# Kernel tuning notes

Measured on AMD Instinct MI355X. Metric: run time of the kernel, lower is better.

Reference implementation:

```python
import jax, jax.numpy as jnp
import numpy as np

H = 1024          # hid_dim
SEQ = 149         # input tokens (cls makes 150)
B = 128           # batch
WIN = 20          # local attention band half-width (hard-coded in module)


def _pe_table(n, d):
    # ConstantPE with period=1: position = 2*pi*arange(n)
    pos = 2.0 * np.pi * np.arange(n, dtype=np.float64)[:, None]
    div = np.exp(np.arange(0, d, 2, dtype=np.float64) * (-np.log(10000.0) / d))
    pe = np.zeros((n, d), dtype=np.float32)
    pe[:, 0::2] = np.sin(pos * div)
    pe[:, 1::2] = np.cos(pos * div)
    return jnp.asarray(pe)


def _band_mask(n, w=WIN):
    # True where attention is DISALLOWED (matches src_mask == 1)
    r = np.arange(n)[:, None]
    c = np.arange(n)[None, :]
    allowed = (c >= np.maximum(r - w, 0)) & (c < r + w)
    allowed[0, :] = True  # cls row attends everywhere
    return jnp.asarray(~allowed)


def _layer_norm(x, g, b, eps=1e-5):
    m = jnp.mean(x, axis=-1, keepdims=True)
    v = jnp.var(x, axis=-1, keepdims=True)
    return (x - m) * jax.lax.rsqrt(v + eps) * g + b


def setup_inputs() -> dict:
    key = jax.random.key(0)
    ks = jax.random.split(key, 8)
    s = 0.02
    return {
        "z": jax.random.normal(ks[0], (SEQ, B, H), jnp.float32),
        "cls_token": jax.random.normal(ks[1], (1, H), jnp.float32),
        "ln_g": jnp.ones((H,), jnp.float32),
        "ln_b": jnp.zeros((H,), jnp.float32),
        "w_qkv": jax.random.normal(ks[2], (H, 3 * H), jnp.float32) * s,
        "b_qkv": jnp.zeros((3 * H,), jnp.float32),
        "w_o": jax.random.normal(ks[3], (H, H), jnp.float32) * s,
        "b_o": jnp.zeros((H,), jnp.float32),
        "w_m1": jax.random.normal(ks[4], (H, H), jnp.float32) * s,
        "b_m1": jnp.zeros((H,), jnp.float32),
        "w_m2": jax.random.normal(ks[5], (H, H), jnp.float32) * s,
        "b_m2": jnp.zeros((H,), jnp.float32),
    }


def reference(z, cls_token, ln_g, ln_b, w_qkv, b_qkv, w_o, b_o, w_m1, b_m1, w_m2, b_m2):
    S1 = z.shape[0] + 1  # tokens incl. cls
    pe = _pe_table(S1, H)          # (S1, H)
    neg_mask = _band_mask(S1)      # (S1, S1) bool, True = masked

    x = jnp.swapaxes(z, 0, 1)                                   # (B, S, H)
    cls = jnp.broadcast_to(cls_token[None], (x.shape[0], 1, H))  # (B, 1, H)
    x = jnp.concatenate([cls, x], axis=1)                        # (B, S1, H)
    x = _layer_norm(x + pe[None], ln_g, ln_b)

    qkv = x @ w_qkv + b_qkv
    q, k, v = jnp.split(qkv, 3, axis=-1)

    attn = jnp.einsum("bqh,bkh->bqk", q, k) / jnp.sqrt(jnp.float32(H))
    attn = jnp.where(neg_mask[None], jnp.float32(-1e10), attn)
    attn = jax.nn.softmax(attn, axis=-1)

    sa = jnp.einsum("bqk,bkh->bqh", attn, v) @ w_o + b_o
    zsa = _layer_norm(x + sa, ln_g, ln_b)

    mlp = jax.nn.gelu(zsa @ w_m1 + b_m1, approximate=False) @ w_m2 + b_m2
    out = zsa + mlp
    return jnp.swapaxes(out, 0, 1)  # (S1, B, H)
```

## Files before the change

### kernel.cpp

```cpp
#include <hip/hip_runtime.h>
#include <math.h>

#define HD 1024
#define S1 150
#define BATCH 128
#define MTOK (S1 * BATCH)
#define WIN 20
#define QKVLD (3 * HD)

typedef unsigned short bf16_t;
typedef short s16x8 __attribute__((ext_vector_type(8)));
typedef float f32x4 __attribute__((ext_vector_type(4)));

__device__ __forceinline__ float bf2f(unsigned int u16) {
  return __uint_as_float(u16 << 16);
}
__device__ __forceinline__ unsigned short f2bf(float f) {
  unsigned int u = __float_as_uint(f);
  u += 0x7fff + ((u >> 16) & 1);
  return (unsigned short)(u >> 16);
}

__device__ __forceinline__ float wave_sum(float v) {
#pragma unroll
  for (int o = 32; o; o >>= 1) v += __shfl_down(v, o, 64);
  return v;
}

__device__ __forceinline__ void gload_lds16(const bf16_t* g, bf16_t* l) {
  __builtin_amdgcn_global_load_lds(
      (const __attribute__((address_space(1))) unsigned int*)(unsigned long long)(const void*)g,
      (__attribute__((address_space(3))) unsigned int*)(unsigned int)(unsigned long long)(void*)l,
      16, 0, 0);
}

__global__ __launch_bounds__(256) void transpose_kernel(
    const float* __restrict__ W, bf16_t* __restrict__ WT, int K, int N) {
  __shared__ float t[32][33];
  int n0 = blockIdx.x * 32, k0 = blockIdx.y * 32;
  int tx = threadIdx.x, ty = threadIdx.y;
#pragma unroll
  for (int i = 0; i < 4; i++)
    t[ty + i * 8][tx] = W[(size_t)(k0 + ty + i * 8) * N + n0 + tx];
  __syncthreads();
#pragma unroll
  for (int i = 0; i < 4; i++)
    WT[(size_t)(n0 + ty + i * 8) * K + k0 + tx] = f2bf(t[tx][ty + i * 8]);
}

__global__ void pe_kernel(float* __restrict__ pe) {
  int s = blockIdx.x;
  double pos = 6.283185307179586476925286766559 * (double)s;
  for (int p = threadIdx.x; p < HD / 2; p += blockDim.x) {
    double dv = exp((double)(2 * p) * (-9.210340371976184 / (double)HD));
    double a = pos * dv;
    pe[s * HD + 2 * p] = (float)sin(a);
    pe[s * HD + 2 * p + 1] = (float)cos(a);
  }
}

__global__ __launch_bounds__(256) void build_x_kernel(
    const float* __restrict__ z, const float* __restrict__ cls,
    const float* __restrict__ pe, const float* __restrict__ g,
    const float* __restrict__ be, bf16_t* __restrict__ x) {
  int t = blockIdx.x;
  int b = t / S1, s = t % S1;
  const float* src = (s == 0) ? cls : (z + ((size_t)(s - 1) * BATCH + b) * HD);
  const float* pr = pe + (size_t)s * HD;
  int tid = threadIdx.x;
  float vals[4];
  float sum = 0.f, sq = 0.f;
#pragma unroll
  for (int i = 0; i < 4; i++) {
    int h = tid + i * 256;
    float v = src[h] + pr[h];
    vals[i] = v;
    sum += v;
    sq += v * v;
  }
  __shared__ float shs[4], shq[4];
  __shared__ float sm, sr;
  sum = wave_sum(sum);
  sq = wave_sum(sq);
  int wave = tid >> 6, lane = tid & 63;
  if (!lane) { shs[wave] = sum; shq[wave] = sq; }
  __syncthreads();
  if (!tid) {
    float S = shs[0] + shs[1] + shs[2] + shs[3];
    float Q = shq[0] + shq[1] + shq[2] + shq[3];
    float mean = S * (1.f / HD);
    float var = Q * (1.f / HD) - mean * mean;
    sm = mean;
    sr = rsqrtf(var + 1e-5f);
  }
  __syncthreads();
  float mean = sm, rstd = sr;
  bf16_t* xr = x + (size_t)t * HD;
#pragma unroll
  for (int i = 0; i < 4; i++) {
    int h = tid + i * 256;
    xr[h] = f2bf((vals[i] - mean) * rstd * g[h] + be[h]);
  }
}

__global__ __launch_bounds__(256) void ln_residual_kernel(
    const bf16_t* __restrict__ a, const bf16_t* __restrict__ r,
    const float* __restrict__ g, const float* __restrict__ be,
    bf16_t* __restrict__ out) {
  int t = blockIdx.x;
  int tid = threadIdx.x;
  const bf16_t* ar = a + (size_t)t * QKVLD;
  const bf16_t* rr = r + (size_t)t * HD;
  float vals[4];
  float sum = 0.f, sq = 0.f;
#pragma unroll
  for (int i = 0; i < 4; i++) {
    int h = tid + i * 256;
    float v = bf2f(ar[h]) + bf2f(rr[h]);
    vals[i] = v;
    sum += v;
    sq += v * v;
  }
  __shared__ float shs[4], shq[4];
  __shared__ float sm, sr;
  sum = wave_sum(sum);
  sq = wave_sum(sq);
  int wave = tid >> 6, lane = tid & 63;
  if (!lane) { shs[wave] = sum; shq[wave] = sq; }
  __syncthreads();
  if (!tid) {
    float S = shs[0] + shs[1] + shs[2] + shs[3];
    float Q = shq[0] + shq[1] + shq[2] + shq[3];
    float mean = S * (1.f / HD);
    float var = Q * (1.f / HD) - mean * mean;
    sm = mean;
    sr = rsqrtf(var + 1e-5f);
  }
  __syncthreads();
  float mean = sm, rstd = sr;
  bf16_t* outp = out + (size_t)t * QKVLD;
#pragma unroll
  for (int i = 0; i < 4; i++) {
    int h = tid + i * 256;
    outp[h] = f2bf((vals[i] - mean) * rstd * g[h] + be[h]);
  }
}

template <int EPI>
__global__ __launch_bounds__(512, 2) void gemm256_kernel(
    const bf16_t* __restrict__ A, int lda, const bf16_t* __restrict__ WT,
    const float* __restrict__ bias, bf16_t* __restrict__ C, int ldc,
    const bf16_t* __restrict__ res, float* __restrict__ outf) {
  constexpr int NT = 32;
  __shared__ bf16_t ALDS[4 * 8192];
  __shared__ bf16_t BLDS[4 * 8192];
  int tid = threadIdx.x;
  int w = tid >> 6, lane = tid & 63;
  int wm = w >> 2, wn = w & 3;
  int m0 = blockIdx.y * 256, n0 = blockIdx.x * 256;

  int sr = lane >> 2;
  int scol = ((lane & 3) ^ ((sr >> 1) & 3)) * 8;
  const bf16_t* gA = A + (size_t)(m0 + w * 16 + sr) * lda + scol;
  const bf16_t* gB = WT + (size_t)(n0 + w * 16 + sr) * 1024 + scol;
  bf16_t* lA = ALDS + w * 512;
  bf16_t* lB = BLDS + w * 512;
  size_t ldh = (size_t)128 * lda;

#define STAGE_A(tt)                                                   \
  do {                                                                \
    int bb_ = (tt) & 3;                                               \
    gload_lds16(gA + (tt) * 32, lA + bb_ * 8192);                     \
    gload_lds16(gA + ldh + (tt) * 32, lA + bb_ * 8192 + 4096);        \
  } while (0)
#define STAGE_B(tt)                                                   \
  do {                                                                \
    int bb_ = (tt) & 3;                                               \
    gload_lds16(gB + (tt) * 32, lB + bb_ * 8192);                     \
    gload_lds16(gB + 131072 + (tt) * 32, lB + bb_ * 8192 + 4096);     \
  } while (0)

  int frow = lane & 15;
  int fslot = ((lane >> 4) ^ ((frow >> 1) & 3)) * 8;
  int aoff[8], boff[4];
#pragma unroll
  for (int i = 0; i < 8; i++) aoff[i] = (wm * 8 + i) * 512 + frow * 32 + fslot;
#pragma unroll
  for (int j = 0; j < 4; j++) boff[j] = (wn * 4 + j) * 512 + frow * 32 + fslot;

  f32x4 acc[8][4] = {};

  STAGE_A(0); STAGE_B(0);
  STAGE_A(1); STAGE_B(1);
  STAGE_A(2); STAGE_B(2);

  for (int t = 0; t < NT; ++t) {
    const bf16_t* Ab = ALDS + (t & 3) * 8192;
    const bf16_t* Bb = BLDS + (t & 3) * 8192;
    asm volatile("s_waitcnt vmcnt(8)" ::: "memory");
    __builtin_amdgcn_s_barrier();
    asm volatile("" ::: "memory");
    bool pf = (t + 3 < NT);
    if (pf) STAGE_A(t + 3);
    s16x8 af[8], b0, b1;
#pragma unroll
    for (int i = 0; i < 8; i++) af[i] = *(const s16x8*)(Ab + aoff[i]);
    b0 = *(const s16x8*)(Bb + boff[0]);
    b1 = *(const s16x8*)(Bb + boff[1]);
    __builtin_amdgcn_s_setprio(1);
#pragma unroll
    for (int i = 0; i < 8; i++) {
      acc[i][0] = __builtin_amdgcn_mfma_f32_16x16x32_bf16(af[i], b0, acc[i][0], 0, 0, 0);
      acc[i][1] = __builtin_amdgcn_mfma_f32_16x16x32_bf16(af[i], b1, acc[i][1], 0, 0, 0);
    }
    __builtin_amdgcn_s_setprio(0);
    if (pf) STAGE_B(t + 3);
    b0 = *(const s16x8*)(Bb + boff[2]);
    b1 = *(const s16x8*)(Bb + boff[3]);
    __builtin_amdgcn_s_setprio(1);
#pragma unroll
    for (int i = 0; i < 8; i++) {
      acc[i][2] = __builtin_amdgcn_mfma_f32_16x16x32_bf16(af[i], b0, acc[i][2], 0, 0, 0);
      acc[i][3] = __builtin_amdgcn_mfma_f32_16x16x32_bf16(af[i], b1, acc[i][3], 0, 0, 0);
    }
    __builtin_amdgcn_s_setprio(0);
  }
#undef STAGE_A
#undef STAGE_B

  int erow = (lane >> 4) * 4, ecol = lane & 15;
#pragma unroll
  for (int j = 0; j < 4; j++) {
    int n = n0 + wn * 64 + j * 16 + ecol;
    float bb = bias[n];
#pragma unroll
    for (int i = 0; i < 8; i++) {
      int mb = m0 + wm * 128 + i * 16 + erow;
#pragma unroll
      for (int r = 0; r < 4; r++) {
        int m = mb + r;
        float v = acc[i][j][r] + bb;
        if (EPI == 1) v = 0.5f * v * (1.f + erff(v * 0.7071067811865476f));
        if (EPI == 2) {
          int b = m / S1, s = m % S1;
          v += bf2f(res[(size_t)m * QKVLD + n]);
          outf[((size_t)s * BATCH + b) * HD + n] = v;
        } else {
          C[(size_t)m * ldc + n] = f2bf(v);
        }
      }
    }
  }
}

__global__ __launch_bounds__(256) void attn_tile_kernel(bf16_t* __restrict__ qkv) {
  int g = blockIdx.x;
  int xcd = g & 7, tt0 = g >> 3;
  int qt = tt0 % 5, b = xcd + 8 * (tt0 / 5);
  int q0 = qt * 32;

  int lo_col = (qt == 0) ? 0 : (q0 - 20);
  int hi_col = (qt == 0) ? 150 : ((q0 + 51 < 150) ? q0 + 51 : 150);
  int ct0 = lo_col >> 5;
  int cth = (hi_col + 31) >> 5;
  int NCT = cth - ct0;
  int W = NCT * 32;
  int NSUB = NCT * 2;
  int NT = 2 * NSUB;
  int T = NT >> 2;

  __shared__ bf16_t Qs[2 * 32 * 32];
  __shared__ bf16_t Ks[2 * 160 * 32];
  __shared__ float S[32][164];

  int tid = threadIdx.x;
  int w = tid >> 6, lane = tid & 63;

  const bf16_t* kvbase = qkv + (size_t)b * S1 * QKVLD;

  int sr = lane >> 2;
  int scol = ((lane & 3) ^ ((lane >> 3) & 3)) * 8;
  int frow = lane & 15;
  int fslot = (((lane >> 4) ^ ((frow >> 1) & 3))) * 8;

  f32x4 acc[5] = {};

  int U1 = 2 + NSUB;

  for (int k0 = 0; k0 < 1024; k0 += 64) {
    for (int uu = w; uu < 2 * U1; uu += 4) {
      int p = (uu >= U1) ? 1 : 0;
      int ur = uu - p * U1;
      int col = k0 + p * 32 + scol;
      if (ur < 2) {
        int qrow = q0 + ur * 16 + sr;
        if (qrow > 149) qrow = 149;
        gload_lds16(kvbase + (size_t)qrow * QKVLD + col,
                    Qs + p * 1024 + (ur * 16) * 32);
      } else {
        int cr0 = (ur - 2) * 16;
        int cg = ct0 * 32 + cr0 + sr;
        if (cg > 149) cg = 149;
        gload_lds16(kvbase + (size_t)cg * QKVLD + HD + col,
                    Ks + p * 5120 + cr0 * 32);
      }
    }
    __syncthreads();
    s16x8 af0[2], af1[2];
#pragma unroll
    for (int p = 0; p < 2; p++) {
      af0[p] = *(const s16x8*)(Qs + p * 1024 + (0 * 16 + frow) * 32 + fslot);
      af1[p] = *(const s16x8*)(Qs + p * 1024 + (1 * 16 + frow) * 32 + fslot);
    }
#pragma unroll
    for (int t = 0; t < 5; t++) {
      if (t < T) {
        int tidt = w + t * 4;
        int qs = (tidt >= NSUB) ? 1 : 0;
        int cs = tidt - qs * NSUB;
#pragma unroll
        for (int p = 0; p < 2; p++) {
          s16x8 bf = *(const s16x8*)(Ks + p * 5120 + (cs * 16 + frow) * 32 + fslot);
          s16x8 a = qs ? af1[p] : af0[p];
          acc[t] = __builtin_amdgcn_mfma_f32_16x16x32_bf16(a, bf, acc[t], 0, 0, 0);
        }
      }
    }
    __syncthreads();
  }

  int erow = (lane >> 4) * 4, ecol = lane & 15;
#pragma unroll
  for (int t = 0; t < 5; t++) {
    if (t < T) {
      int tidt = w + t * 4;
      int qs = (tidt >= NSUB) ? 1 : 0;
      int cs = tidt - qs * NSUB;
#pragma unroll
      for (int r = 0; r < 4; r++) {
        int qrel = qs * 16 + erow + r;
        int crel = cs * 16 + ecol;
        int qg = q0 + qrel, cg = ct0 * 32 + crel;
        bool ok = (qg < 150) && (cg < 150) &&
                  ((qg == 0) || (cg >= qg - WIN && cg < qg + WIN));
        S[qrel][crel] = ok ? acc[t][r] * 0.03125f : -1e30f;
      }
    }
  }
  __syncthreads();

  {
    int q = tid >> 3, j = tid & 7;
    float m = -1e30f;
    for (int c = j; c < W; c += 8) m = fmaxf(m, S[q][c]);
#pragma unroll
    for (int o = 1; o < 8; o <<= 1) m = fmaxf(m, __shfl_xor(m, o, 64));
    float s = 0.f;
    for (int c = j; c < W; c += 8) {
      float e = __expf(S[q][c] - m);
      S[q][c] = e;
      s += e;
    }
#pragma unroll
    for (int o = 1; o < 8; o <<= 1) s += __shfl_xor(s, o, 64);
    float inv = 1.f / s;
    for (int c = j; c < W; c += 8) S[q][c] *= inv;
  }
  __syncthreads();

  int qg0 = q0 + 8 * w;
  if (qg0 < 150) {
    int lo = (qt == 0 && w == 0) ? 0 : ((qg0 - WIN > 0) ? qg0 - WIN : 0);
    int hi = (qt == 0 && w == 0) ? 150 : ((qg0 + 27 < 150) ? qg0 + 27 : 150);
    int c0base = ct0 * 32;
#pragma unroll
    for (int hp = 0; hp < 2; hp++) {
      int hb = hp * 512 + lane * 8;
      float a[8][8];
#pragma unroll
      for (int qi = 0; qi < 8; qi++)
#pragma unroll
        for (int e = 0; e < 8; e++) a[qi][e] = 0.f;
      const bf16_t* vb = kvbase + 2 * HD + hb;
      for (int c = lo; c < hi; ++c) {
        uint4 vv = *(const uint4*)(vb + (size_t)c * QKVLD);
        float vf[8];
        vf[0] = __uint_as_float(vv.x << 16);
        vf[1] = __uint_as_float(vv.x & 0xffff0000u);
        vf[2] = __uint_as_float(vv.y << 16);
        vf[3] = __uint_as_float(vv.y & 0xffff0000u);
        vf[4] = __uint_as_float(vv.z << 16);
        vf[5] = __uint_as_float(vv.z & 0xffff0000u);
        vf[6] = __uint_as_float(vv.w << 16);
        vf[7] = __uint_as_float(vv.w & 0xffff0000u);
        int crel = c - c0base;
#pragma unroll
        for (int qi = 0; qi < 8; qi++) {
          float p = S[8 * w + qi][crel];
#pragma unroll
          for (int e = 0; e < 8; e++) a[qi][e] += p * vf[e];
        }
      }
#pragma unroll
      for (int qi = 0; qi < 8; qi++) {
        int qg = qg0 + qi;
        if (qg < 150) {
          uint4 pk;
          pk.x = (unsigned int)f2bf(a[qi][0]) | ((unsigned int)f2bf(a[qi][1]) << 16);
          pk.y = (unsigned int)f2bf(a[qi][2]) | ((unsigned int)f2bf(a[qi][3]) << 16);
          pk.z = (unsigned int)f2bf(a[qi][4]) | ((unsigned int)f2bf(a[qi][5]) << 16);
          pk.w = (unsigned int)f2bf(a[qi][6]) | ((unsigned int)f2bf(a[qi][7]) << 16);
          *(uint4*)(qkv + ((size_t)b * S1 + qg) * QKVLD + hb) = pk;
        }
      }
    }
  }
}

extern "C" void kernel_launch(void* const* d_in, const int* in_sizes, int n_in,
                              void* d_out, int out_size, void* d_ws, size_t ws_size,
                              hipStream_t stream) {
  (void)in_sizes; (void)n_in; (void)out_size; (void)ws_size;
  const float* z = (const float*)d_in[0];
  const float* cls = (const float*)d_in[1];
  const float* ln_g = (const float*)d_in[2];
  const float* ln_b = (const float*)d_in[3];
  const float* w_qkv = (const float*)d_in[4];
  const float* b_qkv = (const float*)d_in[5];
  const float* w_o = (const float*)d_in[6];
  const float* b_o = (const float*)d_in[7];
  const float* w_m1 = (const float*)d_in[8];
  const float* b_m1 = (const float*)d_in[9];
  const float* w_m2 = (const float*)d_in[10];
  const float* b_m2 = (const float*)d_in[11];

  char* wsb = (char*)d_ws;
  bf16_t* wt_m2 = (bf16_t*)wsb;
  float* pe = (float*)(wsb + 2097152);
  bf16_t* qkv = (bf16_t*)(wsb + 2097152 + 614400);

  char* outb = (char*)d_out;
  bf16_t* x = (bf16_t*)outb;
  bf16_t* wt_qkv = (bf16_t*)(outb + 39321600);
  bf16_t* wt_o = (bf16_t*)(outb + 45613056);
  bf16_t* wt_m1 = (bf16_t*)(outb + 47710208);

  bf16_t* av = qkv;
  bf16_t* sa = qkv + HD;
  bf16_t* zsa = qkv + 2 * HD;
  bf16_t* h1 = qkv;
  float* out = (float*)d_out;

  transpose_kernel<<<dim3(96, 32), dim3(32, 8), 0, stream>>>(w_qkv, wt_qkv, HD, 3 * HD);
  transpose_kernel<<<dim3(32, 32), dim3(32, 8), 0, stream>>>(w_o, wt_o, HD, HD);
  transpose_kernel<<<dim3(32, 32), dim3(32, 8), 0, stream>>>(w_m1, wt_m1, HD, HD);
  transpose_kernel<<<dim3(32, 32), dim3(32, 8), 0, stream>>>(w_m2, wt_m2, HD, HD);
  pe_kernel<<<S1, 256, 0, stream>>>(pe);
  build_x_kernel<<<MTOK, 256, 0, stream>>>(z, cls, pe, ln_g, ln_b, x);
  gemm256_kernel<0><<<dim3(12, 75), 512, 0, stream>>>(
      x, HD, wt_qkv, b_qkv, qkv, QKVLD, nullptr, nullptr);
  attn_tile_kernel<<<640, 256, 0, stream>>>(qkv);
  gemm256_kernel<0><<<dim3(4, 75), 512, 0, stream>>>(
      av, QKVLD, wt_o, b_o, sa, QKVLD, nullptr, nullptr);
  ln_residual_kernel<<<MTOK, 256, 0, stream>>>(sa, x, ln_g, ln_b, zsa);
  gemm256_kernel<1><<<dim3(4, 75), 512, 0, stream>>>(
      zsa, QKVLD, wt_m1, b_m1, h1, QKVLD, nullptr, nullptr);
  gemm256_kernel<2><<<dim3(4, 75), 512, 0, stream>>>(
      h1, QKVLD, wt_m2, b_m2, nullptr, 0, zsa, out);
}
```

Before: 743.9 us.

## Rework GEMM mainloop into 8-phase double-buffered pipeline, merge weight transposes

```diff
diff --git a/kernel.cpp b/kernel.cpp
--- a/kernel.cpp
+++ b/kernel.cpp
@@ -34,10 +34,27 @@
       16, 0, 0);
 }
 
-__global__ __launch_bounds__(256) void transpose_kernel(
-    const float* __restrict__ W, bf16_t* __restrict__ WT, int K, int N) {
+__global__ __launch_bounds__(256) void transpose_all_kernel(
+    const float* __restrict__ w_qkv, bf16_t* __restrict__ wt_qkv,
+    const float* __restrict__ w_o, bf16_t* __restrict__ wt_o,
+    const float* __restrict__ w_m1, bf16_t* __restrict__ wt_m1,
+    const float* __restrict__ w_m2, bf16_t* __restrict__ wt_m2) {
+  int g = blockIdx.x;
+  const float* W;
+  bf16_t* WT;
+  int N, bx, by;
+  if (g < 3072) {
+    W = w_qkv; WT = wt_qkv; N = 3072;
+    bx = g % 96; by = g / 96;
+  } else {
+    int r = g - 3072;
+    int which = r >> 10, l = r & 1023;
+    bx = l & 31; by = l >> 5; N = 1024;
+    W = (which == 0) ? w_o : (which == 1) ? w_m1 : w_m2;
+    WT = (which == 0) ? wt_o : (which == 1) ? wt_m1 : wt_m2;
+  }
   __shared__ float t[32][33];
-  int n0 = blockIdx.x * 32, k0 = blockIdx.y * 32;
+  int n0 = bx * 32, k0 = by * 32;
   int tx = threadIdx.x, ty = threadIdx.y;
 #pragma unroll
   for (int i = 0; i < 4; i++)
@@ -45,7 +62,7 @@
   __syncthreads();
 #pragma unroll
   for (int i = 0; i < 4; i++)
-    WT[(size_t)(n0 + ty + i * 8) * K + k0 + tx] = f2bf(t[tx][ty + i * 8]);
+    WT[(size_t)(n0 + ty + i * 8) * 1024 + k0 + tx] = f2bf(t[tx][ty + i * 8]);
 }
 
 __global__ void pe_kernel(float* __restrict__ pe) {
@@ -147,66 +164,72 @@
 }
 
 template <int EPI>
-__global__ __launch_bounds__(512, 2) void gemm256_kernel(
+__global__ __launch_bounds__(512) void gemm8p_kernel(
     const bf16_t* __restrict__ A, int lda, const bf16_t* __restrict__ WT,
     const float* __restrict__ bias, bf16_t* __restrict__ C, int ldc,
     const bf16_t* __restrict__ res, float* __restrict__ outf) {
-  constexpr int NT = 32;
-  __shared__ bf16_t ALDS[4 * 8192];
-  __shared__ bf16_t BLDS[4 * 8192];
+  constexpr int NT = 16;
+  __shared__ bf16_t As[32768];
+  __shared__ bf16_t Bs[32768];
   int tid = threadIdx.x;
   int w = tid >> 6, lane = tid & 63;
   int wm = w >> 2, wn = w & 3;
   int m0 = blockIdx.y * 256, n0 = blockIdx.x * 256;
 
-  int sr = lane >> 2;
-  int scol = ((lane & 3) ^ ((sr >> 1) & 3)) * 8;
-  const bf16_t* gA = A + (size_t)(m0 + w * 16 + sr) * lda + scol;
-  const bf16_t* gB = WT + (size_t)(n0 + w * 16 + sr) * 1024 + scol;
-  bf16_t* lA = ALDS + w * 512;
-  bf16_t* lB = BLDS + w * 512;
-  size_t ldh = (size_t)128 * lda;
-
-#define STAGE_A(tt)                                                   \
-  do {                                                                \
-    int bb_ = (tt) & 3;                                               \
-    gload_lds16(gA + (tt) * 32, lA + bb_ * 8192);                     \
-    gload_lds16(gA + ldh + (tt) * 32, lA + bb_ * 8192 + 4096);        \
+  int srow = lane >> 2;
+  int scol = ((lane & 3) ^ ((lane >> 3) & 3)) * 8;
+  const bf16_t* gA = A + (size_t)(m0 + w * 16 + srow) * lda + scol;
+  const bf16_t* gB = WT + (size_t)(n0 + w * 16 + srow) * 1024 + scol;
+  const size_t ldhA = (size_t)128 * lda;
+  const size_t ldhB = (size_t)128 * 1024;
+  bf16_t* AsW = As + w * 512;
+  bf16_t* BsW = Bs + w * 512;
+
+#define STAGE_A(tt, pp)                                         \
+  do {                                                          \
+    const bf16_t* s_ = gA + (tt) * 64 + (pp) * 32;              \
+    bf16_t* d_ = AsW + ((tt) & 1) * 16384 + (pp) * 8192;        \
+    gload_lds16(s_, d_);                                        \
+    gload_lds16(s_ + ldhA, d_ + 4096);                          \
   } while (0)
-#define STAGE_B(tt)                                                   \
-  do {                                                                \
-    int bb_ = (tt) & 3;                                               \
-    gload_lds16(gB + (tt) * 32, lB + bb_ * 8192);                     \
-    gload_lds16(gB + 131072 + (tt) * 32, lB + bb_ * 8192 + 4096);     \
+#define STAGE_B(tt, pp)                                         \
+  do {                                                          \
+    const bf16_t* s_ = gB + (tt) * 64 + (pp) * 32;              \
+    bf16_t* d_ = BsW + ((tt) & 1) * 16384 + (pp) * 8192;        \
+    gload_lds16(s_, d_);                                        \
+    gload_lds16(s_ + ldhB, d_ + 4096);                          \
   } while (0)
 
   int frow = lane & 15;
   int fslot = ((lane >> 4) ^ ((frow >> 1) & 3)) * 8;
   int aoff[8], boff[4];
 #pragma unroll
-  for (int i = 0; i < 8; i++) aoff[i] = (wm * 8 + i) * 512 + frow * 32 + fslot;
-#pragma unroll
-  for (int j = 0; j < 4; j++) boff[j] = (wn * 4 + j) * 512 + frow * 32 + fslot;
+  for (int i = 0; i < 8; i++)
+    aoff[i] = (wm * 128 + i * 16 + frow) * 32 + fslot;
+#pragma unroll
+  for (int j = 0; j < 4; j++)
+    boff[j] = (wn * 64 + j * 16 + frow) * 32 + fslot;
 
   f32x4 acc[8][4] = {};
 
-  STAGE_A(0); STAGE_B(0);
-  STAGE_A(1); STAGE_B(1);
-  STAGE_A(2); STAGE_B(2);
-
+  STAGE_A(0, 0); STAGE_A(0, 1); STAGE_B(0, 0); STAGE_B(0, 1); STAGE_A(1, 0);
+  asm volatile("s_waitcnt vmcnt(4)" ::: "memory");
+  __builtin_amdgcn_s_barrier();
+
+#pragma unroll 2
   for (int t = 0; t < NT; ++t) {
-    const bf16_t* Ab = ALDS + (t & 3) * 8192;
-    const bf16_t* Bb = BLDS + (t & 3) * 8192;
-    asm volatile("s_waitcnt vmcnt(8)" ::: "memory");
-    __builtin_amdgcn_s_barrier();
-    asm volatile("" ::: "memory");
-    bool pf = (t + 3 < NT);
-    if (pf) STAGE_A(t + 3);
+    const bf16_t* Ab = As + (t & 1) * 16384;
+    const bf16_t* Bb = Bs + (t & 1) * 16384;
     s16x8 af[8], b0, b1;
+
 #pragma unroll
     for (int i = 0; i < 8; i++) af[i] = *(const s16x8*)(Ab + aoff[i]);
     b0 = *(const s16x8*)(Bb + boff[0]);
     b1 = *(const s16x8*)(Bb + boff[1]);
+    if (t < NT - 1) STAGE_A(t + 1, 1);
+    __builtin_amdgcn_s_barrier();
+    asm volatile("s_waitcnt lgkmcnt(0)" ::: "memory");
+    __builtin_amdgcn_sched_barrier(0);
     __builtin_amdgcn_s_setprio(1);
 #pragma unroll
     for (int i = 0; i < 8; i++) {
@@ -214,9 +237,14 @@
       acc[i][1] = __builtin_amdgcn_mfma_f32_16x16x32_bf16(af[i], b1, acc[i][1], 0, 0, 0);
     }
     __builtin_amdgcn_s_setprio(0);
-    if (pf) STAGE_B(t + 3);
+    __builtin_amdgcn_s_barrier();
+
     b0 = *(const s16x8*)(Bb + boff[2]);
     b1 = *(const s16x8*)(Bb + boff[3]);
+    if (t < NT - 1) STAGE_B(t + 1, 0);
+    __builtin_amdgcn_s_barrier();
+    asm volatile("s_waitcnt lgkmcnt(0)" ::: "memory");
+    __builtin_amdgcn_sched_barrier(0);
     __builtin_amdgcn_s_setprio(1);
 #pragma unroll
     for (int i = 0; i < 8; i++) {
@@ -224,6 +252,49 @@
       acc[i][3] = __builtin_amdgcn_mfma_f32_16x16x32_bf16(af[i], b1, acc[i][3], 0, 0, 0);
     }
     __builtin_amdgcn_s_setprio(0);
+    if (t < NT - 1) {
+      asm volatile("s_waitcnt vmcnt(6)" ::: "memory");
+    } else {
+      asm volatile("s_waitcnt vmcnt(0)" ::: "memory");
+    }
+    __builtin_amdgcn_s_barrier();
+
+#pragma unroll
+    for (int i = 0; i < 8; i++) af[i] = *(const s16x8*)(Ab + 8192 + aoff[i]);
+    b0 = *(const s16x8*)(Bb + 8192 + boff[0]);
+    b1 = *(const s16x8*)(Bb + 8192 + boff[1]);
+    if (t < NT - 1) STAGE_B(t + 1, 1);
+    __builtin_amdgcn_s_barrier();
+    asm volatile("s_waitcnt lgkmcnt(0)" ::: "memory");
+    __builtin_amdgcn_sched_barrier(0);
+    __builtin_amdgcn_s_setprio(1);
+#pragma unroll
+    for (int i = 0; i < 8; i++) {
+      acc[i][0] = __builtin_amdgcn_mfma_f32_16x16x32_bf16(af[i], b0, acc[i][0], 0, 0, 0);
+      acc[i][1] = __builtin_amdgcn_mfma_f32_16x16x32_bf16(af[i], b1, acc[i][1], 0, 0, 0);
+    }
+    __builtin_amdgcn_s_setprio(0);
+    __builtin_amdgcn_s_barrier();
+
+    b0 = *(const s16x8*)(Bb + 8192 + boff[2]);
+    b1 = *(const s16x8*)(Bb + 8192 + boff[3]);
+    if (t < NT - 2) STAGE_A(t + 2, 0);
+    __builtin_amdgcn_s_barrier();
+    asm volatile("s_waitcnt lgkmcnt(0)" ::: "memory");
+    __builtin_amdgcn_sched_barrier(0);
+    __builtin_amdgcn_s_setprio(1);
+#pragma unroll
+    for (int i = 0; i < 8; i++) {
+      acc[i][2] = __builtin_amdgcn_mfma_f32_16x16x32_bf16(af[i], b0, acc[i][2], 0, 0, 0);
+      acc[i][3] = __builtin_amdgcn_mfma_f32_16x16x32_bf16(af[i], b1, acc[i][3], 0, 0, 0);
+    }
+    __builtin_amdgcn_s_setprio(0);
+    if (t < NT - 2) {
+      asm volatile("s_waitcnt vmcnt(4)" ::: "memory");
+    } else if (t == NT - 2) {
+      asm volatile("s_waitcnt vmcnt(2)" ::: "memory");
+    }
+    __builtin_amdgcn_s_barrier();
   }
 #undef STAGE_A
 #undef STAGE_B
@@ -451,20 +522,18 @@
   bf16_t* h1 = qkv;
   float* out = (float*)d_out;
 
-  transpose_kernel<<<dim3(96, 32), dim3(32, 8), 0, stream>>>(w_qkv, wt_qkv, HD, 3 * HD);
-  transpose_kernel<<<dim3(32, 32), dim3(32, 8), 0, stream>>>(w_o, wt_o, HD, HD);
-  transpose_kernel<<<dim3(32, 32), dim3(32, 8), 0, stream>>>(w_m1, wt_m1, HD, HD);
-  transpose_kernel<<<dim3(32, 32), dim3(32, 8), 0, stream>>>(w_m2, wt_m2, HD, HD);
+  transpose_all_kernel<<<6144, dim3(32, 8), 0, stream>>>(
+      w_qkv, wt_qkv, w_o, wt_o, w_m1, wt_m1, w_m2, wt_m2);
   pe_kernel<<<S1, 256, 0, stream>>>(pe);
   build_x_kernel<<<MTOK, 256, 0, stream>>>(z, cls, pe, ln_g, ln_b, x);
-  gemm256_kernel<0><<<dim3(12, 75), 512, 0, stream>>>(
+  gemm8p_kernel<0><<<dim3(12, 75), 512, 0, stream>>>(
       x, HD, wt_qkv, b_qkv, qkv, QKVLD, nullptr, nullptr);
   attn_tile_kernel<<<640, 256, 0, stream>>>(qkv);
-  gemm256_kernel<0><<<dim3(4, 75), 512, 0, stream>>>(
+  gemm8p_kernel<0><<<dim3(4, 75), 512, 0, stream>>>(
       av, QKVLD, wt_o, b_o, sa, QKVLD, nullptr, nullptr);
   ln_residual_kernel<<<MTOK, 256, 0, stream>>>(sa, x, ln_g, ln_b, zsa);
-  gemm256_kernel<1><<<dim3(4, 75), 512, 0, stream>>>(
+  gemm8p_kernel<1><<<dim3(4, 75), 512, 0, stream>>>(
       zsa, QKVLD, wt_m1, b_m1, h1, QKVLD, nullptr, nullptr);
-  gemm256_kernel<2><<<dim3(4, 75), 512, 0, stream>>>(
+  gemm8p_kernel<2><<<dim3(4, 75), 512, 0, stream>>>(
       h1, QKVLD, wt_m2, b_m2, nullptr, 0, zsa, out);
 }
```

Measured after the change: 739.3 us. Within noise of the previous version (-0.6%).
